# Kernel optimization log

Hardware: AMD Instinct MI355X
Metric: run time of the kernel (lower is better)

The kernel has to match this reference:

```python
import jax, jax.numpy as jnp
import numpy as np
from jax import lax

B, C, H, W = 8, 1024, 64, 48
A = 9  # anchors per location

def _conv(x, w, b, pad):
    y = lax.conv_general_dilated(x, w, (1, 1), pad,
                                 dimension_numbers=('NCHW', 'OIHW', 'NCHW'))
    return y + b[None, :, None, None]

def setup_inputs() -> dict:
    key = jax.random.key(0)
    ks = jax.random.split(key, 12)
    base_feat = jax.random.normal(ks[0], (B, C, H, W), dtype=jnp.float32)
    W_conv = jax.random.normal(ks[1], (512, C, 3, 3), dtype=jnp.float32) * 0.01
    b_conv = jnp.zeros((512,), jnp.float32)
    W_cls = jax.random.normal(ks[2], (18, 512, 1, 1), dtype=jnp.float32) * 0.01
    b_cls = jnp.zeros((18,), jnp.float32)
    W_bbox = jax.random.normal(ks[3], (36, 512, 1, 1), dtype=jnp.float32) * 0.01
    b_bbox = jnp.zeros((36,), jnp.float32)
    # anchor-target-layer outputs (data-dependent assignment) provided as inputs
    rpn_label = (jax.random.randint(ks[4], (B, A * H * W), 0, 3) - 1).astype(jnp.int32)  # {-1,0,1}
    rpn_bbox_targets = jax.random.normal(ks[5], (B, 36, H, W), dtype=jnp.float32) * 0.1
    rpn_bbox_inside_weights = (jax.random.uniform(ks[6], (B, 36, H, W)) < 0.25).astype(jnp.float32)
    rpn_bbox_outside_weights = jax.random.uniform(ks[7], (B, 36, H, W), dtype=jnp.float32) * 0.01
    return {"base_feat": base_feat, "W_conv": W_conv, "b_conv": b_conv,
            "W_cls": W_cls, "b_cls": b_cls, "W_bbox": W_bbox, "b_bbox": b_bbox,
            "rpn_label": rpn_label, "rpn_bbox_targets": rpn_bbox_targets,
            "rpn_bbox_inside_weights": rpn_bbox_inside_weights,
            "rpn_bbox_outside_weights": rpn_bbox_outside_weights}

def reference(base_feat, W_conv, b_conv, W_cls, b_cls, W_bbox, b_bbox,
              rpn_label, rpn_bbox_targets, rpn_bbox_inside_weights,
              rpn_bbox_outside_weights):
    # RPN head: 3x3 conv + relu, then 1x1 cls / bbox heads
    rpn_conv1 = jax.nn.relu(_conv(base_feat, W_conv, b_conv, ((1, 1), (1, 1))))
    cls_score = _conv(rpn_conv1, W_cls, b_cls, ((0, 0), (0, 0)))   # [B,18,H,W]
    bbox_pred = _conv(rpn_conv1, W_bbox, b_bbox, ((0, 0), (0, 0)))  # [B,36,H,W]
    # reshape to [B,2,A*H,W], softmax over the 2-way fg/bg axis, reshape back
    score_rs = cls_score.reshape(B, 2, A * H, W)
    prob_rs = jax.nn.softmax(score_rs, axis=1)
    rpn_cls_prob = prob_rs.reshape(B, 18, H, W)
    # classification loss: permute(0,2,3,1).view(-1,2), keep labels != -1
    logits = score_rs.transpose(0, 2, 3, 1).reshape(-1, 2)
    label = rpn_label.reshape(-1)
    valid = (label != -1).astype(logits.dtype)
    logp = jax.nn.log_softmax(logits, axis=-1)
    lbl = jnp.clip(label, 0, 1)
    nll = -jnp.take_along_axis(logp, lbl[:, None].astype(jnp.int32), axis=1)[:, 0]
    rpn_loss_cls = jnp.sum(nll * valid) / jnp.maximum(jnp.sum(valid), 1.0)
    # smooth-L1 box loss, sigma=3, summed over dims [1,2,3], mean over batch
    sigma2 = 9.0
    in_diff = rpn_bbox_inside_weights * (bbox_pred - rpn_bbox_targets)
    abs_d = jnp.abs(in_diff)
    sign = lax.stop_gradient((abs_d < 1.0 / sigma2).astype(abs_d.dtype))
    in_loss = in_diff * in_diff * (sigma2 / 2.0) * sign + (abs_d - 0.5 / sigma2) * (1.0 - sign)
    rpn_loss_box = jnp.mean(jnp.sum(rpn_bbox_outside_weights * in_loss, axis=(1, 2, 3)))
    return rpn_cls_prob, bbox_pred, rpn_loss_cls, rpn_loss_box
```

## Files before the change

### kernel.cpp

```cpp
#include <hip/hip_runtime.h>
#include <stdint.h>

#define B_    8
#define CIN   1024
#define H_    64
#define W_    48
#define OC    512
#define HW    3072
#define NPOS  24576
#define K9    9216
#define HP    66
#define WP    50

typedef __attribute__((ext_vector_type(8))) __bf16 bf16x8;
typedef __attribute__((ext_vector_type(4))) float  float4_t;
typedef __attribute__((ext_vector_type(4))) unsigned short ushort4_t;
typedef __attribute__((ext_vector_type(8))) int int8v;
typedef __attribute__((ext_vector_type(4))) int int4v;

__device__ __forceinline__ unsigned short f2bf(float x) {
  union { float f; unsigned u; } v; v.f = x;
  unsigned r = v.u + 0x7FFFu + ((v.u >> 16) & 1u);
  return (unsigned short)(r >> 16);
}

__device__ __forceinline__ unsigned int pack4_fp8(float a, float b, float c, float d) {
  int w = __builtin_amdgcn_cvt_pk_fp8_f32(a, b, 0, false);
  w = __builtin_amdgcn_cvt_pk_fp8_f32(c, d, w, true);
  return (unsigned int)w;
}

__device__ __forceinline__ void async16(const void* g, void* l) {
  __builtin_amdgcn_global_load_lds(
      (const __attribute__((address_space(1))) unsigned int*)g,
      (__attribute__((address_space(3))) unsigned int*)l, 16, 0, 0);
}

__device__ __forceinline__ float wave_sum(float v) {
  for (int o = 32; o > 0; o >>= 1) v += __shfl_down(v, o, 64);
  return v;
}

__global__ void prep_fused(const float* __restrict__ x, const float* __restrict__ Wc,
                           const float* __restrict__ Wcls, const float* __restrict__ Wbb,
                           unsigned char* __restrict__ xt, unsigned char* __restrict__ Wa,
                           unsigned short* __restrict__ Wh, float* __restrict__ accbuf) {
  __shared__ float smem[9216];
  int bid = blockIdx.x, t = threadIdx.x;
  if (bid < 4096) {
    int cx = bid & 7, h = (bid >> 3) & 63, b = bid >> 9;
    float* tile = smem;
    const float* src = x + ((long)(b * CIN + cx * 128) * H_ + h) * W_;
    for (int it = 0; it < 6; ++it) {
      int e = it * 256 + t;
      int cl = e / 12, w4 = e % 12;
      float4_t v = *(const float4_t*)&src[(long)cl * HW + w4 * 4];
      int base = cl * 49 + w4 * 4;
      tile[base] = v.x; tile[base + 1] = v.y; tile[base + 2] = v.z; tile[base + 3] = v.w;
    }
    __syncthreads();
    unsigned char* dst = xt + ((long)(b * HP + h + 1) * WP + 1) * CIN + cx * 128;
    for (int it = 0; it < 6; ++it) {
      int e = it * 256 + t;
      int w = e >> 5, g = e & 31;
      float v0 = tile[(g * 4 + 0) * 49 + w] * 16.f;
      float v1 = tile[(g * 4 + 1) * 49 + w] * 16.f;
      float v2 = tile[(g * 4 + 2) * 49 + w] * 16.f;
      float v3 = tile[(g * 4 + 3) * 49 + w] * 16.f;
      *(unsigned int*)&dst[(long)w * CIN + g * 4] = pack4_fp8(v0, v1, v2, v3);
    }
  } else if (bid < 4608) {
    int o = bid - 4096;
    float* lw = smem;
    const float* src = Wc + (long)o * K9;
    for (int i = 0; i < 9; ++i)
      *(float4_t*)&lw[i * 1024 + t * 4] = *(const float4_t*)&src[i * 1024 + t * 4];
    __syncthreads();
    unsigned char* dst = Wa + (long)o * K9;
    int c = t * 4;
    for (int off = 0; off < 9; ++off) {
      float v0 = lw[(c + 0) * 9 + off] * 512.f;
      float v1 = lw[(c + 1) * 9 + off] * 512.f;
      float v2 = lw[(c + 2) * 9 + off] * 512.f;
      float v3 = lw[(c + 3) * 9 + off] * 512.f;
      *(unsigned int*)&dst[off * 1024 + c] = pack4_fp8(v0, v1, v2, v3);
    }
  } else if (bid < 4640) {
    int e = (bid - 4608) * 1024 + t * 4;
    int m = e >> 9, c = e & 511;
    float v0 = 0.f, v1 = 0.f, v2 = 0.f, v3 = 0.f;
    if (m < 18) {
      const float* s = Wcls + m * 512 + c;
      v0 = s[0]; v1 = s[1]; v2 = s[2]; v3 = s[3];
    } else if (m < 54) {
      const float* s = Wbb + (m - 18) * 512 + c;
      v0 = s[0]; v1 = s[1]; v2 = s[2]; v3 = s[3];
    }
    ushort4_t pk; pk.x = f2bf(v0); pk.y = f2bf(v1); pk.z = f2bf(v2); pk.w = f2bf(v3);
    *(ushort4_t*)&Wh[e] = pk;
    if (bid == 4608 && t < 4) accbuf[t] = 0.f;
  } else {
    int bid2 = bid - 4640;
    int b = bid2 / 66, h = bid2 % 66;
    unsigned char* base = xt + (long)(b * 66 + h) * 50 * 1024;
    int4v z = {};
    if (h == 0 || h == 65) {
      for (int i = t; i < 3200; i += 256) *(int4v*)(base + (long)i * 16) = z;
    } else if (t < 128) {
      int which = t >> 6, off = t & 63;
      *(int4v*)(base + (long)which * 49 * 1024 + (long)off * 16) = z;
    }
  }
}

#define BKF 128
__global__ __launch_bounds__(256, 2)
void conv_gemm(const unsigned char* __restrict__ Wa, const unsigned char* __restrict__ xt,
               const float* __restrict__ bias, unsigned short* __restrict__ conv1) {
  __shared__ unsigned char As[2][128 * BKF];
  __shared__ unsigned char Bs[2][128 * BKF];
  int t = threadIdx.x;
  int lane = t & 63, wv = t >> 6;
  int m0 = blockIdx.y * 128;
  int n0 = blockIdx.x * 128;
  const unsigned char* aSrc[4];
  const unsigned char* bSrc[4];
  for (int s = 0; s < 4; ++s) {
    int c = s * 256 + t;
    int r = c >> 3;
    int q = (c & 7) ^ (r & 7);
    aSrc[s] = Wa + (long)(m0 + r) * K9 + q * 16;
    int n = n0 + r; int b = n / HW; int rem = n % HW; int h = rem / W_; int w = rem % W_;
    bSrc[s] = xt + ((long)(b * HP + h) * WP + w) * CIN + q * 16;
  }
  float4_t acc[4][4] = {};
  int wm = wv >> 1, wn = wv & 1;
  int quad = lane >> 4, col = lane & 15;

  auto stage = [&](int buf, int kt) {
    int off = kt >> 3;
    int dy = off / 3, dx = off % 3;
    long boff = (long)(dy * WP + dx) * CIN + (kt & 7) * 128;
    long aoff = (long)kt * 128;
    for (int s = 0; s < 4; ++s)
      async16(aSrc[s] + aoff, &As[buf][s * 4096 + wv * 1024]);
    for (int s = 0; s < 4; ++s)
      async16(bSrc[s] + boff, &Bs[buf][s * 4096 + wv * 1024]);
  };

  auto compute = [&](int buf) {
    int8v af[4], bfr[4];
    for (int i = 0; i < 4; ++i) {
      int r = wm * 64 + i * 16 + col;
      int rb = r * 128, x7 = r & 7;
      int4v lo = *(const int4v*)&As[buf][rb + (((quad * 2 + 0) ^ x7) << 4)];
      int4v hi = *(const int4v*)&As[buf][rb + (((quad * 2 + 1) ^ x7) << 4)];
      af[i] = (int8v){lo.x, lo.y, lo.z, lo.w, hi.x, hi.y, hi.z, hi.w};
    }
    for (int j = 0; j < 4; ++j) {
      int r = wn * 64 + j * 16 + col;
      int rb = r * 128, x7 = r & 7;
      int4v lo = *(const int4v*)&Bs[buf][rb + (((quad * 2 + 0) ^ x7) << 4)];
      int4v hi = *(const int4v*)&Bs[buf][rb + (((quad * 2 + 1) ^ x7) << 4)];
      bfr[j] = (int8v){lo.x, lo.y, lo.z, lo.w, hi.x, hi.y, hi.z, hi.w};
    }
    __builtin_amdgcn_s_setprio(1);
    for (int i = 0; i < 4; ++i)
      for (int j = 0; j < 4; ++j)
        acc[i][j] = __builtin_amdgcn_mfma_scale_f32_16x16x128_f8f6f4(
            af[i], bfr[j], acc[i][j], 0, 0, 0, 0x76767676, 0, 0x7B7B7B7B);
    __builtin_amdgcn_s_setprio(0);
    __builtin_amdgcn_sched_barrier(0);
    asm volatile("s_waitcnt lgkmcnt(0)\n\ts_barrier" ::: "memory");
  };

  stage(0, 0);
#pragma unroll 1
  for (int kt = 0; kt < 72; kt += 2) {
    stage(1, kt + 1);
    asm volatile("s_waitcnt vmcnt(8)\n\ts_barrier" ::: "memory");
    compute(0);
    if (kt + 2 < 72) {
      stage(0, kt + 2);
      asm volatile("s_waitcnt vmcnt(8)\n\ts_barrier" ::: "memory");
    } else {
      asm volatile("s_waitcnt vmcnt(0)\n\ts_barrier" ::: "memory");
    }
    compute(1);
  }

  for (int i = 0; i < 4; ++i) {
    int mb = m0 + wm * 64 + i * 16 + quad * 4;
    float b0 = bias[mb + 0], b1 = bias[mb + 1], b2 = bias[mb + 2], b3 = bias[mb + 3];
    for (int j = 0; j < 4; ++j) {
      int n = n0 + wn * 64 + j * 16 + col;
      ushort4_t pk;
      pk.x = f2bf(fmaxf(acc[i][j].x + b0, 0.f));
      pk.y = f2bf(fmaxf(acc[i][j].y + b1, 0.f));
      pk.z = f2bf(fmaxf(acc[i][j].z + b2, 0.f));
      pk.w = f2bf(fmaxf(acc[i][j].w + b3, 0.f));
      *(ushort4_t*)&conv1[(long)n * 512 + mb] = pk;
    }
  }
}

__global__ __launch_bounds__(256, 2)
void head_gemm(const unsigned short* __restrict__ Wh, const unsigned short* __restrict__ conv1,
               const float* __restrict__ b_cls, const float* __restrict__ b_bbox,
               float* __restrict__ cls_ws, float* __restrict__ out_bbox) {
  __shared__ unsigned short As[64 * 128];
  __shared__ unsigned short Bs[64 * 128];
  int t = threadIdx.x;
  int lane = t & 63, wv = t >> 6;
  int n0 = blockIdx.x * 64;
  int quad = lane >> 4, col = lane & 15;
  const unsigned short* aS[4];
  const unsigned short* bS[4];
  for (int p = 0; p < 4; ++p) {
    int c = p * 256 + t;
    int r = c >> 4;
    int q = (c & 15) ^ (r & 15);
    aS[p] = Wh + (long)r * 512 + q * 8;
    bS[p] = conv1 + (long)(n0 + r) * 512 + q * 8;
  }
  float4_t acc[4] = {};
  for (int kt = 0; kt < 4; ++kt) {
    long koff = (long)kt * 128;
    __syncthreads();
    for (int p = 0; p < 4; ++p) async16(aS[p] + koff, &As[p * 2048 + wv * 512]);
    for (int p = 0; p < 4; ++p) async16(bS[p] + koff, &Bs[p * 2048 + wv * 512]);
    __syncthreads();
    for (int ks = 0; ks < 4; ++ks) {
      int rn = wv * 16 + col;
      bf16x8 bfr = *(const bf16x8*)&Bs[rn * 128 + (((ks * 4 + quad) ^ (rn & 15)) << 3)];
      for (int i = 0; i < 4; ++i) {
        int r = i * 16 + col;
        bf16x8 af = *(const bf16x8*)&As[r * 128 + (((ks * 4 + quad) ^ (r & 15)) << 3)];
        acc[i] = __builtin_amdgcn_mfma_f32_16x16x32_bf16(af, bfr, acc[i], 0, 0, 0);
      }
    }
  }
  int n = n0 + wv * 16 + col;
  int b = n / HW; int rem = n % HW;
  for (int i = 0; i < 4; ++i) {
    for (int r = 0; r < 4; ++r) {
      int m = i * 16 + quad * 4 + r;
      float v = acc[i][r];
      if (m < 18) {
        cls_ws[(long)(b * 18 + m) * HW + rem] = v + b_cls[m];
      } else if (m < 54) {
        out_bbox[(long)(b * 36 + (m - 18)) * HW + rem] = v + b_bbox[m - 18];
      }
    }
  }
}

__global__ void loss_fused(const float* __restrict__ cls, const int* __restrict__ label,
                           float* __restrict__ prob,
                           const float* __restrict__ pred, const float* __restrict__ tgt,
                           const float* __restrict__ iw, const float* __restrict__ ow,
                           float* __restrict__ acc) {
  int lane = threadIdx.x & 63, wv = threadIdx.x >> 6;
  __shared__ float red[8];
  if (blockIdx.x < 864) {
    int idx = blockIdx.x * 256 + threadIdx.x;
    int b = idx / 27648; int r = idx % 27648;
    int a = r / HW; int r2 = r % HW;
    long i0 = (long)(b * 18 + a) * HW + r2;
    long i1 = i0 + (long)9 * HW;
    float x0 = cls[i0], x1 = cls[i1];
    float mx = fmaxf(x0, x1);
    float e0 = __expf(x0 - mx), e1 = __expf(x1 - mx);
    float s = e0 + e1;
    prob[i0] = e0 / s;
    prob[i1] = e1 / s;
    int lb = label[idx];
    float nll = 0.f, val = 0.f;
    if (lb != -1) {
      val = 1.f;
      float xl = (lb > 0) ? x1 : x0;
      nll = -(xl - mx - __logf(s));
    }
    nll = wave_sum(nll);
    val = wave_sum(val);
    if (lane == 0) { red[wv] = nll; red[4 + wv] = val; }
    __syncthreads();
    if (threadIdx.x == 0) {
      atomicAdd(&acc[0], red[0] + red[1] + red[2] + red[3]);
      atomicAdd(&acc[1], red[4] + red[5] + red[6] + red[7]);
    }
  } else {
    int bid = blockIdx.x - 864;
    float s = 0.f;
    const long total = (long)B_ * 36 * HW;
    for (long i = (long)bid * 256 + threadIdx.x; i < total; i += (long)1728 * 256) {
      float d = iw[i] * (pred[i] - tgt[i]);
      float ad = fabsf(d);
      float l = (ad < (1.f / 9.f)) ? d * d * 4.5f : ad - (1.f / 18.f);
      s += ow[i] * l;
    }
    s = wave_sum(s);
    if (lane == 0) red[wv] = s;
    __syncthreads();
    if (threadIdx.x == 0) atomicAdd(&acc[2], red[0] + red[1] + red[2] + red[3]);
  }
}

__global__ void finalize(const float* __restrict__ acc, float* __restrict__ out) {
  if (threadIdx.x == 0) {
    out[0] = acc[0] / fmaxf(acc[1], 1.f);
    out[1] = acc[2] / (float)B_;
  }
}

extern "C" void kernel_launch(void* const* d_in, const int* in_sizes, int n_in,
                              void* d_out, int out_size, void* d_ws, size_t ws_size,
                              hipStream_t stream) {
  const float* base_feat = (const float*)d_in[0];
  const float* W_conv    = (const float*)d_in[1];
  const float* b_conv    = (const float*)d_in[2];
  const float* W_cls     = (const float*)d_in[3];
  const float* b_cls     = (const float*)d_in[4];
  const float* W_bbox    = (const float*)d_in[5];
  const float* b_bbox    = (const float*)d_in[6];
  const int*   rpn_label = (const int*)d_in[7];
  const float* bb_tgt    = (const float*)d_in[8];
  const float* bb_iw     = (const float*)d_in[9];
  const float* bb_ow     = (const float*)d_in[10];

  float* out = (float*)d_out;
  float* out_cls_prob = out;
  float* out_bbox     = out + 442368;
  float* out_scalars  = out + 442368 + 884736;

  size_t off = 0;
  auto alloc = [&](size_t bytes) {
    void* p = (char*)d_ws + off;
    off = (off + bytes + 255) & ~(size_t)255;
    return p;
  };
  const size_t XT_BYTES = (size_t)B_ * HP * WP * CIN;
  unsigned char*  xt    = (unsigned char*)alloc(XT_BYTES);
  unsigned char*  Wa    = (unsigned char*)alloc((size_t)OC * K9);
  unsigned short* conv1 = (unsigned short*)alloc((size_t)NPOS * OC * 2);
  unsigned short* Wh    = (unsigned short*)alloc((size_t)64 * 512 * 2);
  float* cls_ws         = (float*)alloc((size_t)B_ * 18 * HW * 4);
  float* accbuf         = (float*)alloc(16);

  prep_fused<<<5168, 256, 0, stream>>>(base_feat, W_conv, W_cls, W_bbox, xt, Wa, Wh, accbuf);
  conv_gemm<<<dim3(192, 4), 256, 0, stream>>>(Wa, xt, b_conv, conv1);
  head_gemm<<<384, 256, 0, stream>>>(Wh, conv1, b_cls, b_bbox, cls_ws, out_bbox);
  loss_fused<<<2592, 256, 0, stream>>>(cls_ws, rpn_label, out_cls_prob,
                                       out_bbox, bb_tgt, bb_iw, bb_ow, accbuf);
  finalize<<<1, 64, 0, stream>>>(accbuf, out_scalars);
}
```

Measured before the change: 374.2 us.

## Widen conv GEMM N-tile to 192 and single-buffer A with in-loop prefetch

The FP8 conv GEMM tile grows from 128x128 to 128x192 per block, giving each wave a 4x6 MFMA sub-tile. This raises arithmetic intensity and cuts the grid from 768 to 512 blocks. B stays double-buffered while A is single-buffered and refilled after fragments are read into registers, which keeps LDS within budget (16KB+48KB). The catch is more accumulator registers, fewer blocks across the CUs (possible wave-quantization loss), and an extra barrier per k-step.

```diff
diff --git a/kernel.cpp b/kernel.cpp
--- a/kernel.cpp
+++ b/kernel.cpp
@@ -113,87 +113,91 @@
   }
 }
 
-#define BKF 128
 __global__ __launch_bounds__(256, 2)
 void conv_gemm(const unsigned char* __restrict__ Wa, const unsigned char* __restrict__ xt,
                const float* __restrict__ bias, unsigned short* __restrict__ conv1) {
-  __shared__ unsigned char As[2][128 * BKF];
-  __shared__ unsigned char Bs[2][128 * BKF];
+  __shared__ unsigned char As_[128 * 128];
+  __shared__ unsigned char Bs_[2][192 * 128];
   int t = threadIdx.x;
   int lane = t & 63, wv = t >> 6;
   int m0 = blockIdx.y * 128;
-  int n0 = blockIdx.x * 128;
+  int n0 = blockIdx.x * 192;
   const unsigned char* aSrc[4];
-  const unsigned char* bSrc[4];
+  const unsigned char* bSrc[6];
   for (int s = 0; s < 4; ++s) {
     int c = s * 256 + t;
     int r = c >> 3;
     int q = (c & 7) ^ (r & 7);
     aSrc[s] = Wa + (long)(m0 + r) * K9 + q * 16;
+  }
+  for (int p = 0; p < 6; ++p) {
+    int c = p * 256 + t;
+    int r = c >> 3;
+    int q = (c & 7) ^ (r & 7);
     int n = n0 + r; int b = n / HW; int rem = n % HW; int h = rem / W_; int w = rem % W_;
-    bSrc[s] = xt + ((long)(b * HP + h) * WP + w) * CIN + q * 16;
-  }
-  float4_t acc[4][4] = {};
+    bSrc[p] = xt + ((long)(b * HP + h) * WP + w) * CIN + q * 16;
+  }
+  float4_t acc[4][6] = {};
   int wm = wv >> 1, wn = wv & 1;
   int quad = lane >> 4, col = lane & 15;
 
-  auto stage = [&](int buf, int kt) {
+  auto stageA = [&](int kt) {
+    long aoff = (long)kt * 128;
+    for (int s = 0; s < 4; ++s)
+      async16(aSrc[s] + aoff, &As_[s * 4096 + wv * 1024]);
+  };
+  auto stageB = [&](int buf, int kt) {
     int off = kt >> 3;
     int dy = off / 3, dx = off % 3;
     long boff = (long)(dy * WP + dx) * CIN + (kt & 7) * 128;
-    long aoff = (long)kt * 128;
-    for (int s = 0; s < 4; ++s)
-      async16(aSrc[s] + aoff, &As[buf][s * 4096 + wv * 1024]);
-    for (int s = 0; s < 4; ++s)
-      async16(bSrc[s] + boff, &Bs[buf][s * 4096 + wv * 1024]);
+    for (int p = 0; p < 6; ++p)
+      async16(bSrc[p] + boff, &Bs_[buf][p * 4096 + wv * 1024]);
   };
 
-  auto compute = [&](int buf) {
-    int8v af[4], bfr[4];
+  stageA(0);
+  stageB(0, 0);
+#pragma unroll 1
+  for (int kt = 0; kt < 72; ++kt) {
+    if (kt + 1 < 72) {
+      stageB((kt + 1) & 1, kt + 1);
+      asm volatile("s_waitcnt vmcnt(6)\n\ts_barrier" ::: "memory");
+    } else {
+      asm volatile("s_waitcnt vmcnt(0)\n\ts_barrier" ::: "memory");
+    }
+    const unsigned char* Bcur = Bs_[kt & 1];
+    int8v af[4], bfr[6];
     for (int i = 0; i < 4; ++i) {
       int r = wm * 64 + i * 16 + col;
       int rb = r * 128, x7 = r & 7;
-      int4v lo = *(const int4v*)&As[buf][rb + (((quad * 2 + 0) ^ x7) << 4)];
-      int4v hi = *(const int4v*)&As[buf][rb + (((quad * 2 + 1) ^ x7) << 4)];
+      int4v lo = *(const int4v*)&As_[rb + (((quad * 2 + 0) ^ x7) << 4)];
+      int4v hi = *(const int4v*)&As_[rb + (((quad * 2 + 1) ^ x7) << 4)];
       af[i] = (int8v){lo.x, lo.y, lo.z, lo.w, hi.x, hi.y, hi.z, hi.w};
     }
-    for (int j = 0; j < 4; ++j) {
-      int r = wn * 64 + j * 16 + col;
+    for (int j = 0; j < 6; ++j) {
+      int r = wn * 96 + j * 16 + col;
       int rb = r * 128, x7 = r & 7;
-      int4v lo = *(const int4v*)&Bs[buf][rb + (((quad * 2 + 0) ^ x7) << 4)];
-      int4v hi = *(const int4v*)&Bs[buf][rb + (((quad * 2 + 1) ^ x7) << 4)];
+      int4v lo = *(const int4v*)&Bcur[rb + (((quad * 2 + 0) ^ x7) << 4)];
+      int4v hi = *(const int4v*)&Bcur[rb + (((quad * 2 + 1) ^ x7) << 4)];
       bfr[j] = (int8v){lo.x, lo.y, lo.z, lo.w, hi.x, hi.y, hi.z, hi.w};
     }
+    asm volatile("s_waitcnt lgkmcnt(0)\n\ts_barrier" ::: "memory");
+    __builtin_amdgcn_sched_barrier(0);
+    if (kt + 1 < 72) stageA(kt + 1);
+    __builtin_amdgcn_sched_barrier(0);
     __builtin_amdgcn_s_setprio(1);
     for (int i = 0; i < 4; ++i)
-      for (int j = 0; j < 4; ++j)
+      for (int j = 0; j < 6; ++j)
         acc[i][j] = __builtin_amdgcn_mfma_scale_f32_16x16x128_f8f6f4(
             af[i], bfr[j], acc[i][j], 0, 0, 0, 0x76767676, 0, 0x7B7B7B7B);
     __builtin_amdgcn_s_setprio(0);
     __builtin_amdgcn_sched_barrier(0);
-    asm volatile("s_waitcnt lgkmcnt(0)\n\ts_barrier" ::: "memory");
-  };
-
-  stage(0, 0);
-#pragma unroll 1
-  for (int kt = 0; kt < 72; kt += 2) {
-    stage(1, kt + 1);
-    asm volatile("s_waitcnt vmcnt(8)\n\ts_barrier" ::: "memory");
-    compute(0);
-    if (kt + 2 < 72) {
-      stage(0, kt + 2);
-      asm volatile("s_waitcnt vmcnt(8)\n\ts_barrier" ::: "memory");
-    } else {
-      asm volatile("s_waitcnt vmcnt(0)\n\ts_barrier" ::: "memory");
-    }
-    compute(1);
   }
 
   for (int i = 0; i < 4; ++i) {
     int mb = m0 + wm * 64 + i * 16 + quad * 4;
     float b0 = bias[mb + 0], b1 = bias[mb + 1], b2 = bias[mb + 2], b3 = bias[mb + 3];
-    for (int j = 0; j < 4; ++j) {
-      int n = n0 + wn * 64 + j * 16 + col;
+    for (int j = 0; j < 6; ++j) {
+      int n = n0 + wn * 96 + j * 16 + col;
       ushort4_t pk;
       pk.x = f2bf(fmaxf(acc[i][j].x + b0, 0.f));
       pk.y = f2bf(fmaxf(acc[i][j].y + b1, 0.f));
@@ -348,7 +352,7 @@
   float* accbuf         = (float*)alloc(16);
 
   prep_fused<<<5168, 256, 0, stream>>>(base_feat, W_conv, W_cls, W_bbox, xt, Wa, Wh, accbuf);
-  conv_gemm<<<dim3(192, 4), 256, 0, stream>>>(Wa, xt, b_conv, conv1);
+  conv_gemm<<<dim3(128, 4), 256, 0, stream>>>(Wa, xt, b_conv, conv1);
   head_gemm<<<384, 256, 0, stream>>>(Wh, conv1, b_cls, b_bbox, cls_ws, out_bbox);
   loss_fused<<<2592, 256, 0, stream>>>(cls_ws, rpn_label, out_cls_prob,
                                        out_bbox, bb_tgt, bb_iw, bb_ow, accbuf);
```

Result: faster. 342.5 us (-8.5%).
